# Performance work log

Hardware: AMD Instinct MI355X
Metric: run time of the kernel (lower is better)

## Reference

```python
import jax, jax.numpy as jnp
import numpy as np

# Config (matches init_kwargs)
HQ, HKV, HD, WIN = 16, 4, 128, 512  # query heads, kv heads, head_dim, sliding window


def setup_inputs() -> dict:
    key = jax.random.key(0)
    k0, k1, k2, k3, k4 = jax.random.split(key, 5)
    B, S, D = 1, 8192, 2048
    std = 0.02
    hidden_states = jax.random.normal(k0, (B, S, D), jnp.float32)
    Wq = jax.random.normal(k1, (D, HQ * HD), jnp.float32) * std
    Wk = jax.random.normal(k2, (D, HKV * HD), jnp.float32) * std
    Wv = jax.random.normal(k3, (D, HKV * HD), jnp.float32) * std
    Wo = jax.random.normal(k4, (HQ * HD, D), jnp.float32) * std
    return {"hidden_states": hidden_states, "Wq": Wq, "Wk": Wk, "Wv": Wv, "Wo": Wo}


def _sliding_window_attention(q, k, v, win):
    # block i attend to keys of blocks i-1 and i -> scores [B,H,nb,W,2W].
    B, H, S, hd = q.shape
    W = win
    nb = S // W
    qb = q.reshape(B, H, nb, W, hd)
    kpad = jnp.pad(k, ((0, 0), (0, 0), (W, 0), (0, 0)))
    vpad = jnp.pad(v, ((0, 0), (0, 0), (W, 0), (0, 0)))
    kb = jnp.concatenate([kpad[:, :, :S].reshape(B, H, nb, W, hd),
                          k.reshape(B, H, nb, W, hd)], axis=3)  # [B,H,nb,2W,hd]
    vb = jnp.concatenate([vpad[:, :, :S].reshape(B, H, nb, W, hd),
                          v.reshape(B, H, nb, W, hd)], axis=3)
    # Faithful double-scaling of the source: /sqrt(hd) inside the chunk matmul
    # and again before softmax -> effective /hd.
    scores = jnp.einsum('bhnqd,bhnkd->bhnqk', qb, kb) / jnp.asarray(hd, qb.dtype)
    qi = jnp.arange(W)[:, None]
    ki = jnp.arange(2 * W)[None, :]
    # key local index k maps to global offset (k - W) relative to block start;
    # attend iff 0 <= q_glob - k_glob <= W-1  <=>  q+1 <= k <= q+W
    band = (ki >= qi + 1) & (ki <= qi + W)          # [W, 2W]
    blk = jnp.arange(nb)[:, None, None]
    valid = band[None] & ((blk > 0) | (ki[None] >= W))  # block 0 has no prev keys
    neg = jnp.finfo(scores.dtype).min
    scores = jnp.where(valid[None, None], scores, neg)
    probs = jax.nn.softmax(scores, axis=-1)
    out = jnp.einsum('bhnqk,bhnkd->bhnqd', probs, vb)
    return out.reshape(B, H, S, hd)


def reference(hidden_states, Wq, Wk, Wv, Wo):
    B, S, D = hidden_states.shape
    q = (hidden_states @ Wq).reshape(B, S, HQ, HD).transpose(0, 2, 1, 3)
    k = (hidden_states @ Wk).reshape(B, S, HKV, HD).transpose(0, 2, 1, 3)
    v = (hidden_states @ Wv).reshape(B, S, HKV, HD).transpose(0, 2, 1, 3)
    rep = HQ // HKV
    k = jnp.repeat(k, rep, axis=1)
    v = jnp.repeat(v, rep, axis=1)
    attn = _sliding_window_attention(q, k, v, WIN)      # [B,HQ,S,HD]
    attn = attn.transpose(0, 2, 1, 3).reshape(B, S, HQ * HD)
    return attn @ Wo
```

## Files before the change

kernel.cpp:

```cpp
#include <hip/hip_runtime.h>


typedef __bf16 bf16x8 __attribute__((ext_vector_type(8)));
typedef float f32x4 __attribute__((ext_vector_type(4)));
typedef int v8i __attribute__((ext_vector_type(8)));

__device__ __forceinline__ unsigned short f2bf(float f) {
  unsigned int u = __float_as_uint(f);
  u += 0x7fffu + ((u >> 16) & 1u);
  return (unsigned short)(u >> 16);
}

__device__ __forceinline__ f32x4 mfma16(bf16x8 a, bf16x8 b, f32x4 c) {
  return __builtin_amdgcn_mfma_f32_16x16x32_bf16(a, b, c, 0, 0, 0);
}

__device__ __forceinline__ void async16(void* lds, const void* g) {
  __builtin_amdgcn_global_load_lds(
      (__attribute__((address_space(1))) unsigned int*)g,
      (__attribute__((address_space(3))) unsigned int*)lds, 16, 0, 0);
}


__global__ __launch_bounds__(256) void convert_h_kernel(
    const float* __restrict__ src, unsigned short* __restrict__ dbf,
    unsigned char* __restrict__ d8, int n) {
  int i = (blockIdx.x * 256 + threadIdx.x) * 4;
  if (i < n) {
    float4 f = *(const float4*)(src + i);
    ushort4 o;
    o.x = f2bf(f.x); o.y = f2bf(f.y); o.z = f2bf(f.z); o.w = f2bf(f.w);
    *(ushort4*)(dbf + i) = o;
    int p = __builtin_amdgcn_cvt_pk_fp8_f32(f.x, f.y, 0, 0);
    p = __builtin_amdgcn_cvt_pk_fp8_f32(f.z, f.w, p, 1);
    *(unsigned int*)(d8 + i) = p;
  }
}

__global__ __launch_bounds__(256) void transpose_convert_kernel(
    const float* __restrict__ src, unsigned short* __restrict__ dst,
    int K, int N) {
  __shared__ unsigned short T[64 * 72];
  int kb = blockIdx.y * 64, nb = blockIdx.x * 64;
  int t = threadIdx.x;
  for (int u = t; u < 1024; u += 256) {
    int r = u >> 4, s = u & 15;
    float4 f = *(const float4*)(src + (size_t)(kb + r) * N + nb + s * 4);
    ushort4 o;
    o.x = f2bf(f.x); o.y = f2bf(f.y); o.z = f2bf(f.z); o.w = f2bf(f.w);
    *(ushort4*)&T[r * 72 + s * 4] = o;
  }
  __syncthreads();
  for (int u = t; u < 1024; u += 256) {
    int orow = u >> 4, s = u & 15;
    ushort4 o;
    o.x = T[(s * 4 + 0) * 72 + orow];
    o.y = T[(s * 4 + 1) * 72 + orow];
    o.z = T[(s * 4 + 2) * 72 + orow];
    o.w = T[(s * 4 + 3) * 72 + orow];
    *(ushort4*)(dst + (size_t)(nb + orow) * K + kb + s * 4) = o;
  }
}

__global__ __launch_bounds__(256) void transpose_convert_fp8_kernel(
    const float* __restrict__ src, unsigned char* __restrict__ dst,
    int K, int N) {
  __shared__ unsigned short T[64 * 72];
  int kb = blockIdx.y * 64, nb = blockIdx.x * 64;
  int t = threadIdx.x;
  for (int u = t; u < 1024; u += 256) {
    int r = u >> 4, s = u & 15;
    float4 f = *(const float4*)(src + (size_t)(kb + r) * N + nb + s * 4);
    ushort4 o;
    o.x = f2bf(f.x); o.y = f2bf(f.y); o.z = f2bf(f.z); o.w = f2bf(f.w);
    *(ushort4*)&T[r * 72 + s * 4] = o;
  }
  __syncthreads();
  for (int u = t; u < 1024; u += 256) {
    int orow = u >> 4, s = u & 15;
    float f0 = __uint_as_float((unsigned int)T[(s * 4 + 0) * 72 + orow] << 16);
    float f1 = __uint_as_float((unsigned int)T[(s * 4 + 1) * 72 + orow] << 16);
    float f2 = __uint_as_float((unsigned int)T[(s * 4 + 2) * 72 + orow] << 16);
    float f3 = __uint_as_float((unsigned int)T[(s * 4 + 3) * 72 + orow] << 16);
    int p = __builtin_amdgcn_cvt_pk_fp8_f32(f0, f1, 0, 0);
    p = __builtin_amdgcn_cvt_pk_fp8_f32(f2, f3, p, 1);
    *(unsigned int*)&dst[(size_t)(nb + orow) * K + kb + s * 4] = p;
  }
}

__global__ __launch_bounds__(256) void vtrans_kernel(
    const unsigned short* __restrict__ QKV, unsigned short* __restrict__ VTg) {
  int flat = blockIdx.x * 256 + threadIdx.x;
  int c = flat & 511;
  int s0 = (flat >> 9) * 8;
  unsigned short tmp[8];
  #pragma unroll
  for (int j = 0; j < 8; ++j)
    tmp[j] = QKV[(size_t)(s0 + j) * 3072 + 2560 + c];
  *(uint4*)&VTg[(size_t)c * 8192 + s0] = *(uint4*)tmp;
}


template <bool F32OUT>
__global__ __launch_bounds__(256) void gemm_bt_kernel(
    const unsigned short* __restrict__ A, const unsigned short* __restrict__ BT,
    void* __restrict__ Cp, int M, int ldc, int K) {
  __shared__ unsigned short As[128 * 32];
  __shared__ unsigned short Bs[128 * 32];
  int mb = blockIdx.y * 128, nb = blockIdx.x * 128;
  int tid = threadIdx.x;
  int lane = tid & 63, wv = tid >> 6;
  int wrow = wv >> 1, wcol = wv & 1;
  int lr = lane >> 2, ls = lane & 3;
  int fr = lane & 15, fg = lane >> 4;
  f32x4 acc[4][4] = {};
  for (int k0 = 0; k0 < K; k0 += 32) {
    __syncthreads();
    #pragma unroll
    for (int r = 0; r < 2; ++r) {
      int s = wv * 2 + r;
      async16(&As[s * 512], &A[(size_t)(mb + s * 16 + lr) * K + k0 + ls * 8]);
      async16(&Bs[s * 512], &BT[(size_t)(nb + s * 16 + lr) * K + k0 + ls * 8]);
    }
    __syncthreads();
    bf16x8 a[4], b[4];
    #pragma unroll
    for (int rt = 0; rt < 4; ++rt)
      a[rt] = *(const bf16x8*)&As[(wrow * 64 + rt * 16 + fr) * 32 + fg * 8];
    #pragma unroll
    for (int ct = 0; ct < 4; ++ct)
      b[ct] = *(const bf16x8*)&Bs[(wcol * 64 + ct * 16 + fr) * 32 + fg * 8];
    #pragma unroll
    for (int rt = 0; rt < 4; ++rt)
      #pragma unroll
      for (int ct = 0; ct < 4; ++ct)
        acc[rt][ct] = mfma16(a[rt], b[ct], acc[rt][ct]);
  }
  #pragma unroll
  for (int rt = 0; rt < 4; ++rt)
    #pragma unroll
    for (int ct = 0; ct < 4; ++ct)
      #pragma unroll
      for (int i = 0; i < 4; ++i) {
        int row = mb + wrow * 64 + rt * 16 + fg * 4 + i;
        int col = nb + wcol * 64 + ct * 16 + fr;
        if constexpr (F32OUT)
          ((float*)Cp)[(size_t)row * ldc + col] = acc[rt][ct][i];
        else
          ((unsigned short*)Cp)[(size_t)row * ldc + col] = f2bf(acc[rt][ct][i]);
      }
}


__global__ __launch_bounds__(256) void gemm_qk_fp8_kernel(
    const unsigned char* __restrict__ A8, const unsigned char* __restrict__ B8,
    unsigned short* __restrict__ C, int M, int ldc, int K) {
  __shared__ unsigned char As[128 * 144];
  __shared__ unsigned char Bs[128 * 144];
  int mb = blockIdx.y * 128, nb = blockIdx.x * 128;
  int tid = threadIdx.x;
  int lane = tid & 63, wv = tid >> 6;
  int wrow = wv >> 1, wcol = wv & 1;
  int fr = lane & 15, fg = lane >> 4;
  int srow = tid >> 1, shalf = (tid & 1) * 64;
  f32x4 acc[4][4] = {};
  for (int k0 = 0; k0 < K; k0 += 128) {
    __syncthreads();
    #pragma unroll
    for (int j = 0; j < 4; ++j) {
      *(uint4*)&As[srow * 144 + shalf + j * 16] =
          *(const uint4*)&A8[(size_t)(mb + srow) * K + k0 + shalf + j * 16];
      *(uint4*)&Bs[srow * 144 + shalf + j * 16] =
          *(const uint4*)&B8[(size_t)(nb + srow) * K + k0 + shalf + j * 16];
    }
    __syncthreads();
    v8i a[4], b[4];
    #pragma unroll
    for (int rt = 0; rt < 4; ++rt) {
      int off = (wrow * 64 + rt * 16 + fr) * 144 + fg * 32;
      ((uint4*)&a[rt])[0] = *(const uint4*)&As[off];
      ((uint4*)&a[rt])[1] = *(const uint4*)&As[off + 16];
    }
    #pragma unroll
    for (int ct = 0; ct < 4; ++ct) {
      int off = (wcol * 64 + ct * 16 + fr) * 144 + fg * 32;
      ((uint4*)&b[ct])[0] = *(const uint4*)&Bs[off];
      ((uint4*)&b[ct])[1] = *(const uint4*)&Bs[off + 16];
    }
    #pragma unroll
    for (int rt = 0; rt < 4; ++rt)
      #pragma unroll
      for (int ct = 0; ct < 4; ++ct)
        acc[rt][ct] = __builtin_amdgcn_mfma_scale_f32_16x16x128_f8f6f4(
            a[rt], b[ct], acc[rt][ct], 0, 0,
            0, 0x7F7F7F7F,
            0, 0x7F7F7F7F);
  }
  #pragma unroll
  for (int rt = 0; rt < 4; ++rt)
    #pragma unroll
    for (int ct = 0; ct < 4; ++ct)
      #pragma unroll
      for (int i = 0; i < 4; ++i) {
        int row = mb + wrow * 64 + rt * 16 + fg * 4 + i;
        int col = nb + wcol * 64 + ct * 16 + fr;
        C[(size_t)row * ldc + col] = f2bf(acc[rt][ct][i]);
      }
}


#define SCALE_L2E 0.0112710027f

__global__ __launch_bounds__(512, 2) void attn_kernel(
    const unsigned short* __restrict__ QKV,
    const unsigned short* __restrict__ VTg,
    unsigned short* __restrict__ O) {
  __shared__ unsigned short Ks[64 * 136];
  __shared__ unsigned short VTs[128 * 72];
  __shared__ unsigned short Ps[8 * 32 * 72];
  const int g = blockIdx.y;
  const int qs = blockIdx.x * 64;
  const int tid = threadIdx.x;
  const int lane = tid & 63, w = tid >> 6;
  const int fr = lane & 15, fg = lane >> 4;
  const int hl = w & 3, qh = w >> 2;
  const int h = g * 4 + hl;
  const int kcol = 2048 + g * 128;
  unsigned short* Pw = &Ps[w * 32 * 72];

  bf16x8 qf[2][4];
  #pragma unroll
  for (int qt = 0; qt < 2; ++qt) {
    int qrow = qs + qh * 32 + qt * 16 + fr;
    #pragma unroll
    for (int kk = 0; kk < 4; ++kk)
      qf[qt][kk] = *(const bf16x8*)&QKV[(size_t)qrow * 3072 + h * 128 + kk * 32 + fg * 8];
  }
  f32x4 o_acc[2][8] = {};
  float l_part[2][4] = {};
  const int kb0 = qs >= 512 ? qs - 512 : 0;
  for (int kb = kb0; kb <= qs; kb += 64) {
    __syncthreads();
    #pragma unroll
    for (int it = 0; it < 2; ++it) {
      int u = tid + it * 512;
      int key = u >> 4, seg = u & 15;
      *(uint4*)&Ks[key * 136 + seg * 8] =
          *(const uint4*)&QKV[(size_t)(kb + key) * 3072 + kcol + seg * 8];
    }
    #pragma unroll
    for (int it = 0; it < 2; ++it) {
      int u = tid + it * 512;
      int d = u >> 3, seg = u & 7;
      *(uint4*)&VTs[d * 72 + seg * 8] =
          *(const uint4*)&VTg[(size_t)(g * 128 + d) * 8192 + kb + seg * 8];
    }
    __syncthreads();
    f32x4 s_acc[2][4] = {};
    #pragma unroll
    for (int kt = 0; kt < 4; ++kt) {
      bf16x8 kf[4];
      #pragma unroll
      for (int kk = 0; kk < 4; ++kk)
        kf[kk] = *(const bf16x8*)&Ks[(kt * 16 + fr) * 136 + kk * 32 + fg * 8];
      #pragma unroll
      for (int qt = 0; qt < 2; ++qt)
        #pragma unroll
        for (int kk = 0; kk < 4; ++kk)
          s_acc[qt][kt] = mfma16(qf[qt][kk], kf[kk], s_acc[qt][kt]);
    }
    const bool edge = (kb > qs - 64) || (kb < qs - 448);
    #pragma unroll
    for (int qt = 0; qt < 2; ++qt)
      #pragma unroll
      for (int kt = 0; kt < 4; ++kt)
        #pragma unroll
        for (int i = 0; i < 4; ++i) {
          float p = exp2f(s_acc[qt][kt][i] * SCALE_L2E);
          if (edge) {
            int kg = kb + kt * 16 + fr;
            int qg = qs + qh * 32 + qt * 16 + fg * 4 + i;
            if (kg > qg || kg < qg - 511) p = 0.f;
          }
          l_part[qt][i] += p;
          Pw[(qt * 16 + fg * 4 + i) * 72 + kt * 16 + fr] = f2bf(p);
        }
    bf16x8 af[2][2];
    #pragma unroll
    for (int qt = 0; qt < 2; ++qt)
      #pragma unroll
      for (int kf2 = 0; kf2 < 2; ++kf2)
        af[qt][kf2] = *(const bf16x8*)&Pw[(qt * 16 + fr) * 72 + kf2 * 32 + fg * 8];
    #pragma unroll
    for (int dt = 0; dt < 8; ++dt) {
      bf16x8 vf[2];
      #pragma unroll
      for (int kf2 = 0; kf2 < 2; ++kf2)
        vf[kf2] = *(const bf16x8*)&VTs[(dt * 16 + fr) * 72 + kf2 * 32 + fg * 8];
      #pragma unroll
      for (int qt = 0; qt < 2; ++qt)
        #pragma unroll
        for (int kf2 = 0; kf2 < 2; ++kf2)
          o_acc[qt][dt] = mfma16(af[qt][kf2], vf[kf2], o_acc[qt][dt]);
    }
  }
  #pragma unroll
  for (int qt = 0; qt < 2; ++qt)
    #pragma unroll
    for (int i = 0; i < 4; ++i) {
      float s = l_part[qt][i];
      s += __shfl_xor(s, 1); s += __shfl_xor(s, 2);
      s += __shfl_xor(s, 4); s += __shfl_xor(s, 8);
      l_part[qt][i] = 1.f / s;
    }
  #pragma unroll
  for (int qt = 0; qt < 2; ++qt)
    #pragma unroll
    for (int dt = 0; dt < 8; ++dt)
      #pragma unroll
      for (int i = 0; i < 4; ++i) {
        int row = qs + qh * 32 + qt * 16 + fg * 4 + i;
        O[(size_t)row * 2048 + h * 128 + dt * 16 + fr] =
            f2bf(o_acc[qt][dt][i] * l_part[qt][i]);
      }
}


extern "C" void kernel_launch(void* const* d_in, const int* in_sizes, int n_in,
                              void* d_out, int out_size, void* d_ws, size_t ws_size,
                              hipStream_t stream) {
  const float* h  = (const float*)d_in[0];
  const float* Wq = (const float*)d_in[1];
  const float* Wk = (const float*)d_in[2];
  const float* Wv = (const float*)d_in[3];
  const float* Wo = (const float*)d_in[4];
  float* out = (float*)d_out;
  char* ws = (char*)d_ws;
  const int S = 8192, D = 2048;
  const size_t MB = 1024 * 1024;

  unsigned short* QKV = (unsigned short*)(ws);
  unsigned short* hbf = (unsigned short*)(ws + 48 * MB);
  unsigned short* Ab  = hbf;
  unsigned char*  h8  = (unsigned char*)(ws + 80 * MB);
  unsigned short* VTg = (unsigned short*)(ws + 80 * MB);
  unsigned short* WoT = (unsigned short*)(ws + 88 * MB);
  unsigned char*  W8  = (unsigned char*)(ws + 96 * MB);
  unsigned short* WvT = (unsigned short*)(ws + 96 * MB);

  convert_h_kernel<<<16384, 256, 0, stream>>>(h, hbf, h8, S * D);
  transpose_convert_fp8_kernel<<<dim3(32, 32), 256, 0, stream>>>(Wq, W8, D, 2048);
  transpose_convert_fp8_kernel<<<dim3(8, 32), 256, 0, stream>>>(
      Wk, W8 + (size_t)2048 * 2048, D, 512);
  gemm_qk_fp8_kernel<<<dim3(20, 64), 256, 0, stream>>>(h8, W8, QKV, S, 3072, D);

  transpose_convert_kernel<<<dim3(8, 32), 256, 0, stream>>>(Wv, WvT, D, 512);
  gemm_bt_kernel<false><<<dim3(4, 64), 256, 0, stream>>>(hbf, WvT, QKV + 2560, S, 3072, D);

  vtrans_kernel<<<2048, 256, 0, stream>>>(QKV, VTg);
  transpose_convert_kernel<<<dim3(32, 32), 256, 0, stream>>>(Wo, WoT, D, 2048);
  attn_kernel<<<dim3(128, 4), 512, 0, stream>>>(QKV, VTg, Ab);
  gemm_bt_kernel<true><<<dim3(16, 64), 256, 0, stream>>>(Ab, WoT, out, S, 2048, D);
}
```

Measured before the change: 439.1 us.

## Replace output projection GEMM with 256x256 pipelined 8-wave kernel

Swaps the 128x128 bf16 GEMM used for the output projection for a new 256x256-tile kernel with 8 waves. It double-buffers A and B tiles in 128KB of LDS using async global-to-LDS loads, swizzles LDS addresses, and interleaves staging half-tiles with MFMA phases, raising wave priority around the MFMAs. The aim is more data reuse per tile and better overlap of memory loads with matrix math. The cost is heavy LDS use, only 256 blocks to cover the GPU, and a fixed M/N tiling with no bounds checks.

```diff
diff --git a/kernel.cpp b/kernel.cpp
--- a/kernel.cpp
+++ b/kernel.cpp
@@ -149,6 +149,124 @@
         else
           ((unsigned short*)Cp)[(size_t)row * ldc + col] = f2bf(acc[rt][ct][i]);
       }
+}
+
+
+__global__ __launch_bounds__(512, 2) void gemm8p_oproj_kernel(
+    const unsigned short* __restrict__ A, const unsigned short* __restrict__ BT,
+    float* __restrict__ C, int ldc, int K) {
+  __shared__ unsigned char lds[131072];
+  const int mb = blockIdx.y * 256, nb = blockIdx.x * 256;
+  const int tid = threadIdx.x;
+  const int lane = tid & 63, wv = tid >> 6;
+  const int wm = wv >> 2, wn = wv & 3;
+  const int fr = lane & 15, fg = lane >> 4;
+  const int xr = (fr & 4) ? 32 : 0;
+  const int a_base = (wm * 128 + fr) * 128 + ((fg * 16) ^ xr);
+  const int b_base = (wn * 64 + fr) * 128 + ((fg * 16) ^ xr);
+  const int lsw = (lane * 16) ^ (lane & 32);
+  const int lrow = lsw >> 7, lcol = (lsw & 127) >> 1;
+  const int NT = K >> 6;
+
+  f32x4 acc[8][4] = {};
+  bf16x8 aF[4][2], bF[2][2];
+
+#define FENCE_ asm volatile("" ::: "memory")
+#define BAR_ { FENCE_; __builtin_amdgcn_s_barrier(); FENCE_; }
+#define LGKM0_ asm volatile("s_waitcnt lgkmcnt(0)" ::: "memory")
+#define STAGE_A_(BUFI, T, HALF)                                              \
+  { _Pragma("unroll")                                                        \
+    for (int l = 0; l < 2; ++l) {                                            \
+      int cc = wv * 2 + l;                                                   \
+      int rb = (cc >> 3) * 128 + (HALF) * 64 + (cc & 7) * 8;                 \
+      async16(lds + (BUFI) * 65536 + rb * 128,                               \
+              A + (size_t)(mb + rb + lrow) * K + (T) * 64 + lcol);           \
+    } }
+#define STAGE_B_(BUFI, T, HALF)                                              \
+  { _Pragma("unroll")                                                        \
+    for (int l = 0; l < 2; ++l) {                                            \
+      int cc = wv * 2 + l;                                                   \
+      int rb = (cc >> 2) * 64 + (HALF) * 32 + (cc & 3) * 8;                  \
+      async16(lds + (BUFI) * 65536 + 32768 + rb * 128,                       \
+              BT + (size_t)(nb + rb + lrow) * K + (T) * 64 + lcol);          \
+    } }
+#define LOAD_A_(HALF)                                                        \
+  { _Pragma("unroll")                                                        \
+    for (int q = 0; q < 4; ++q)                                              \
+      _Pragma("unroll")                                                      \
+      for (int kk = 0; kk < 2; ++kk)                                         \
+        aF[q][kk] =                                                          \
+            *(const bf16x8*)&Ab_[a_base + ((HALF)*4 + q) * 2048 + kk * 64]; }
+#define LOAD_B_(HALF)                                                        \
+  { _Pragma("unroll")                                                        \
+    for (int c2 = 0; c2 < 2; ++c2)                                           \
+      _Pragma("unroll")                                                      \
+      for (int kk = 0; kk < 2; ++kk)                                         \
+        bF[c2][kk] =                                                         \
+            *(const bf16x8*)&Bb_[b_base + ((HALF)*2 + c2) * 2048 + kk * 64]; }
+#define MFMA_(RT0, CT0)                                                      \
+  { __builtin_amdgcn_s_setprio(1);                                           \
+    _Pragma("unroll")                                                        \
+    for (int q = 0; q < 4; ++q)                                              \
+      _Pragma("unroll")                                                      \
+      for (int c2 = 0; c2 < 2; ++c2) {                                       \
+        acc[(RT0) + q][(CT0) + c2] =                                         \
+            mfma16(aF[q][0], bF[c2][0], acc[(RT0) + q][(CT0) + c2]);         \
+        acc[(RT0) + q][(CT0) + c2] =                                         \
+            mfma16(aF[q][1], bF[c2][1], acc[(RT0) + q][(CT0) + c2]);         \
+      }                                                                      \
+    __builtin_amdgcn_s_setprio(0); }
+
+  STAGE_A_(0, 0, 0); STAGE_A_(0, 0, 1); STAGE_B_(0, 0, 0); STAGE_B_(0, 0, 1);
+  STAGE_B_(1, 1, 0); STAGE_A_(1, 1, 1);
+  asm volatile("s_waitcnt vmcnt(4)" ::: "memory");
+  BAR_;
+
+  for (int t = 0; t < NT; ++t) {
+    const int cur = t & 1, nxt = cur ^ 1;
+    const unsigned char* Ab_ = lds + cur * 65536;
+    const unsigned char* Bb_ = Ab_ + 32768;
+    LOAD_A_(0); LOAD_B_(0);
+    if (t + 1 < NT) STAGE_A_(nxt, t + 1, 0);
+    BAR_; LGKM0_;
+    MFMA_(0, 0);
+    BAR_;
+    LOAD_A_(1);
+    if (t + 1 < NT) STAGE_B_(nxt, t + 1, 1);
+    BAR_; LGKM0_;
+    MFMA_(4, 0);
+    BAR_;
+    LOAD_B_(1);
+    if (t + 2 < NT) STAGE_B_(cur, t + 2, 0);
+    BAR_; LGKM0_;
+    MFMA_(4, 2);
+    BAR_;
+    LOAD_A_(0);
+    if (t + 2 < NT) STAGE_A_(cur, t + 2, 1);
+    BAR_; LGKM0_;
+    MFMA_(0, 2);
+    asm volatile("s_waitcnt vmcnt(4)" ::: "memory");
+    BAR_;
+  }
+
+  #pragma unroll
+  for (int rt = 0; rt < 8; ++rt)
+    #pragma unroll
+    for (int ct = 0; ct < 4; ++ct)
+      #pragma unroll
+      for (int i = 0; i < 4; ++i) {
+        int row = mb + wm * 128 + rt * 16 + fg * 4 + i;
+        int col = nb + wn * 64 + ct * 16 + fr;
+        C[(size_t)row * ldc + col] = acc[rt][ct][i];
+      }
+#undef FENCE_
+#undef BAR_
+#undef LGKM0_
+#undef STAGE_A_
+#undef STAGE_B_
+#undef LOAD_A_
+#undef LOAD_B_
+#undef MFMA_
 }
 
 
@@ -360,5 +478,5 @@
   vtrans_kernel<<<2048, 256, 0, stream>>>(QKV, VTg);
   transpose_convert_kernel<<<dim3(32, 32), 256, 0, stream>>>(Wo, WoT, D, 2048);
   attn_kernel<<<dim3(128, 4), 512, 0, stream>>>(QKV, VTg, Ab);
-  gemm_bt_kernel<true><<<dim3(16, 64), 256, 0, stream>>>(Ab, WoT, out, S, 2048, D);
-}
+  gemm8p_oproj_kernel<<<dim3(8, 32), 512, 0, stream>>>(Ab, WoT, out, 2048, 2048);
+}
```

Result: faster. 429.4 us (-2.2%).
